# Performance work log

Hardware: AMD Instinct MI355X
Metric: run time of the kernel (lower is better)

The kernel has to match this reference:

```python
import jax, jax.numpy as jnp
import numpy as np

EPS = 1e-08
F_DIM = 512


def setup_inputs() -> dict:
    key = jax.random.key(0)
    ks = jax.random.split(key, 7)
    N, F = 50000, F_DIM
    q = jax.random.normal(ks[0], (N, 1, F), dtype=jnp.float32)
    mu = jax.random.normal(ks[1], (N, 3, F), dtype=jnp.float32)
    # Xavier-ish scaled params
    W_mix = jax.random.normal(ks[2], (2 * F, F), dtype=jnp.float32) * (1.0 / np.sqrt(F))
    W1 = jax.random.normal(ks[3], (F, 2 * F), dtype=jnp.float32) * (1.0 / np.sqrt(2 * F))
    b1 = jnp.zeros((F,), dtype=jnp.float32)
    W2 = jax.random.normal(ks[4], (3 * F, F), dtype=jnp.float32) * (1.0 / np.sqrt(F))
    b2 = jnp.zeros((3 * F,), dtype=jnp.float32)
    return {"q": q, "mu": mu, "W_mix": W_mix, "W1": W1, "b1": b1, "W2": W2, "b2": b2}


def reference(q, mu, W_mix, W1, b1, W2, b2):
    F = q.shape[-1]
    # mu_channel_mix: [N,3,F] @ [F,2F] -> [N,3,2F]
    mu_mix = jnp.einsum('ndf,gf->ndg', mu, W_mix)
    mu_V, mu_W = mu_mix[..., :F], mu_mix[..., F:]
    # vector norm over Cartesian axis -> [N,1,F]
    mu_Vn = jnp.sqrt(jnp.sum(mu_V * mu_V, axis=-2, keepdims=True) + EPS)
    ctx = jnp.concatenate([q, mu_Vn], axis=-1)  # [N,1,2F]
    h = jax.nn.silu(jnp.einsum('nsf,gf->nsg', ctx, W1) + b1)  # [N,1,F]
    x = jnp.einsum('nsf,gf->nsg', h, W2) + b2  # [N,1,3F]
    dq_intra = x[..., :F]
    dmu_intra = x[..., F:2 * F] * mu_W  # broadcast [N,1,F]*[N,3,F]
    dqmu_intra = x[..., 2 * F:] * jnp.sum(mu_V * mu_W, axis=1, keepdims=True)
    q_out = q + dq_intra + dqmu_intra
    mu_out = mu + dmu_intra
    return (q_out, mu_out)
```

## Files before the change

### kernel.cpp

```cpp
#include <hip/hip_runtime.h>
#include <stdint.h>

#define NN 50000
#define QWORDS 25600000

typedef __attribute__((ext_vector_type(8))) short bf16x8;
typedef __attribute__((ext_vector_type(4))) float f32x4;

__device__ __forceinline__ uint32_t f2bf(float x){
  uint32_t u = __builtin_bit_cast(uint32_t, x);
  u += 0x7FFFu + ((u >> 16) & 1u);
  return u >> 16;
}
__device__ __forceinline__ float bf2f(uint32_t b){
  uint32_t u = b << 16;
  return __builtin_bit_cast(float, u);
}
__device__ __forceinline__ void gload16(const uint16_t* g, uint16_t* l){
  __builtin_amdgcn_global_load_lds(
      (const __attribute__((address_space(1))) uint32_t*)g,
      (__attribute__((address_space(3))) uint32_t*)l, 16, 0, 0);
}
__device__ __forceinline__ f32x4 mfma16(bf16x8 a, bf16x8 b, f32x4 c){
  return __builtin_amdgcn_mfma_f32_16x16x32_bf16(a, b, c, 0, 0, 0);
}

#define FENCE() asm volatile("" ::: "memory")

__global__ void k_convert(const float* __restrict__ wmix, const float* __restrict__ w1,
                          const float* __restrict__ w2, uint16_t* __restrict__ dst){
  int i = blockIdx.x * 256 + threadIdx.x;
  int e = i << 2;
  const float* s; int o;
  if (e < 524288)       { s = wmix; o = e; }
  else if (e < 1048576) { s = w1;   o = e - 524288; }
  else                  { s = w2;   o = e - 1048576; }
  f32x4 v = *(const f32x4*)(s + o);
  uint2 pk;
  pk.x = f2bf(v[0]) | (f2bf(v[1]) << 16);
  pk.y = f2bf(v[2]) | (f2bf(v[3]) << 16);
  *(uint2*)(dst + e) = pk;
}

__global__ __launch_bounds__(512, 4)
void k_gemm1(const float* __restrict__ mu, const uint16_t* __restrict__ wmixb,
             uint16_t* __restrict__ qh, float* __restrict__ muW){
  __shared__ uint16_t As[2][12288];
  __shared__ uint16_t Bs[2][8192];
  const int tid  = threadIdx.x;
  const int lane = tid & 63;
  const int w    = tid >> 6;
  const int wn   = w & 3;
  const int wf   = w >> 2;
  const int orig = blockIdx.x;
  const int j    = (orig & 7) * 782 + (orig >> 3);
  const int f0   = (j & 7) * 64;
  const int n0   = (j >> 3) * 64;
  const int lrow = tid >> 4;
  const int lcol = (tid & 15) * 4;

  f32x4 ar[6];
  auto A_LOAD = [&](int ks){
    const int k0 = ks * 64;
    #pragma unroll
    for (int p=0; p<6; ++p){
      int r = p*32 + lrow;
      int d = r >> 6, nrow = r & 63;
      int n = n0 + nrow;
      int g = (n < NN ? n : NN-1)*3 + d;
      ar[p] = *(const f32x4*)(mu + (size_t)g*512 + k0 + lcol);
    }
  };
  auto A_WRITE = [&](int buf){
    #pragma unroll
    for (int p=0; p<6; ++p){
      int r = p*32 + lrow;
      f32x4 v = ar[p];
      uint2 pk;
      pk.x = f2bf(v[0]) | (f2bf(v[1]) << 16);
      pk.y = f2bf(v[2]) | (f2bf(v[3]) << 16);
      *(uint2*)&As[buf][r*64 + (lcol ^ ((r&7)<<3))] = pk;
    }
  };
  auto B_ISSUE = [&](int ks, int buf){
    const int k0 = ks * 64;
    #pragma unroll
    for (int jj=0; jj<2; ++jj){
      int jb = w*2 + jj;
      int row = jb*8 + (lane>>3);
      int g = (row < 64) ? (f0 + row) : (448 + f0 + row);
      int srcc = ((lane&7) ^ ((lane>>3)&7)) * 8;
      gload16(wmixb + (size_t)g*512 + k0 + srcc, &Bs[buf][jb*512]);
    }
  };

  const f32x4 z4 = {0.f,0.f,0.f,0.f};
  f32x4 acc[3][4];
  #pragma unroll
  for (int d=0; d<3; ++d)
    #pragma unroll
    for (int nt=0; nt<4; ++nt) acc[d][nt] = z4;

  A_LOAD(0); B_ISSUE(0, 0); A_WRITE(0);
  for (int ks=0; ks<8; ++ks){
    const int cur = ks & 1;
    __syncthreads();
    if (ks < 7){ A_LOAD(ks+1); B_ISSUE(ks+1, cur^1); }
    #pragma unroll
    for (int kf=0; kf<2; ++kf){
      int kc = kf*32 + (lane>>4)*8;
      bf16x8 af[3];
      #pragma unroll
      for (int d=0; d<3; ++d){
        int r = d*64 + wn*16 + (lane&15);
        af[d] = *(const bf16x8*)&As[cur][r*64 + (kc ^ ((r&7)<<3))];
      }
      #pragma unroll
      for (int nt=0; nt<4; ++nt){
        int ntg = wf*2 + (nt&1) + (nt>>1)*4;
        int rr = ntg*16 + (lane&15);
        bf16x8 bf = *(const bf16x8*)&Bs[cur][rr*64 + (kc ^ ((rr&7)<<3))];
        #pragma unroll
        for (int d=0; d<3; ++d)
          acc[d][nt] = mfma16(bf, af[d], acc[d][nt]);
      }
    }
    if (ks < 7) A_WRITE(cur^1);
  }

  const int rb4 = (lane >> 4) * 4;
  const int nthr = n0 + wn*16 + (lane & 15);
  if (nthr < NN){
    #pragma unroll
    for (int c=0; c<2; ++c){
      int f = f0 + (wf*2 + c)*16 + rb4;
      uint2 pkv, pkd; f32x4 u0v, u1v, u2v;
      uint32_t vb[4], db[4];
      #pragma unroll
      for (int p=0; p<4; ++p){
        float v0 = acc[0][c][p],   v1 = acc[1][c][p],   v2 = acc[2][c][p];
        float u0 = acc[0][c+2][p], u1 = acc[1][c+2][p], u2 = acc[2][c+2][p];
        float vn = sqrtf(v0*v0 + v1*v1 + v2*v2 + 1e-8f);
        float dt = v0*u0 + v1*u1 + v2*u2;
        vb[p] = f2bf(vn); db[p] = f2bf(dt);
        u0v[p] = u0; u1v[p] = u1; u2v[p] = u2;
      }
      pkv.x = vb[0] | (vb[1] << 16); pkv.y = vb[2] | (vb[3] << 16);
      pkd.x = db[0] | (db[1] << 16); pkd.y = db[2] | (db[3] << 16);
      *(uint2*)(qh + (size_t)nthr*1024 + f)       = pkv;
      *(uint2*)(qh + (size_t)nthr*1024 + 512 + f) = pkd;
      size_t mb = (size_t)nthr*1536 + f;
      *(f32x4*)(muW + mb)        = u0v;
      *(f32x4*)(muW + mb + 512)  = u1v;
      *(f32x4*)(muW + mb + 1024) = u2v;
    }
  }
}

__global__ __launch_bounds__(512, 4)
void k_gemm2(const float* __restrict__ q, const uint16_t* __restrict__ w1b,
             const float* __restrict__ b1, uint16_t* __restrict__ qh){
  __shared__ uint16_t A2[2][2048];
  __shared__ uint16_t B2[2][16384];
  const int tid  = threadIdx.x;
  const int lane = tid & 63;
  const int w    = tid >> 6;
  const int wm   = w >> 2;
  const int wn   = w & 3;
  const int n0   = blockIdx.x * 64;

  f32x4 qa;
  auto QA_LOAD = [&](int s){
    int k0 = s*32;
    int row = tid >> 3, ch = tid & 7;
    int nc = (n0 + row < NN) ? n0 + row : NN-1;
    qa = *(const f32x4*)(q + (size_t)nc*512 + k0 + ch*4);
  };
  auto QA_WRITE = [&](int buf){
    int row = tid >> 3, ch = tid & 7;
    uint2 pk;
    pk.x = f2bf(qa[0]) | (f2bf(qa[1]) << 16);
    pk.y = f2bf(qa[2]) | (f2bf(qa[3]) << 16);
    *(uint2*)&A2[buf][row*32 + (((ch>>1) ^ (row&3))<<3) + (ch&1)*4] = pk;
  };
  auto VA_ISSUE = [&](int s, int buf){
    if (w < 4){
      int k0v = (s-16)*32;
      int row = w*16 + (lane>>2);
      int nc = (n0 + row < NN) ? n0 + row : NN-1;
      int srcch = (lane&3) ^ (row&3);
      gload16(qh + (size_t)nc*1024 + k0v + srcch*8, &A2[buf][w*512]);
    }
  };
  auto B_ISSUE = [&](int s, int buf){
    int k0 = s*32;
    #pragma unroll
    for (int jj=0; jj<4; ++jj){
      int j = w*4 + jj;
      int row = j*16 + (lane>>2);
      int srcch = (lane&3) ^ (row&3);
      gload16(w1b + (size_t)row*1024 + k0 + srcch*8, &B2[buf][j*512]);
    }
  };

  const f32x4 z4 = {0.f,0.f,0.f,0.f};
  f32x4 acc2[2][8];
  #pragma unroll
  for (int mt=0; mt<2; ++mt)
    #pragma unroll
    for (int nt=0; nt<8; ++nt) acc2[mt][nt] = z4;

  QA_LOAD(0); B_ISSUE(0, 0); QA_WRITE(0);
  for (int s=0; s<32; ++s){
    const int cur = s & 1;
    __syncthreads();
    if (s < 31){
      if (s+1 < 16) QA_LOAD(s+1); else VA_ISSUE(s+1, cur^1);
      B_ISSUE(s+1, cur^1);
    }
    {
      int kc = (lane>>4)*8;
      bf16x8 a[2];
      #pragma unroll
      for (int mt=0; mt<2; ++mt){
        int r = wm*32 + mt*16 + (lane&15);
        a[mt] = *(const bf16x8*)&A2[cur][r*32 + (kc ^ ((r&3)<<3))];
      }
      #pragma unroll
      for (int nt=0; nt<8; ++nt){
        int rr = wn*128 + nt*16 + (lane&15);
        bf16x8 b = *(const bf16x8*)&B2[cur][rr*32 + (kc ^ ((rr&3)<<3))];
        acc2[0][nt] = mfma16(a[0], b, acc2[0][nt]);
        acc2[1][nt] = mfma16(a[1], b, acc2[1][nt]);
      }
    }
    if (s < 31 && s+1 < 16) QA_WRITE(cur^1);
  }

  const int rb4 = (lane >> 4) * 4;
  #pragma unroll
  for (int nt=0; nt<8; ++nt){
    int col = wn*128 + nt*16 + (lane&15);
    float bb = b1[col];
    #pragma unroll
    for (int mt=0; mt<2; ++mt)
      #pragma unroll
      for (int j=0; j<4; ++j){
        int n = n0 + wm*32 + mt*16 + rb4 + j;
        if (n < NN){
          float x = acc2[mt][nt][j] + bb;
          float sv = x / (1.f + __expf(-x));
          qh[(size_t)n*1024 + col] = (uint16_t)f2bf(sv);
        }
      }
  }
}

__global__ __launch_bounds__(512, 4)
void k_gemm3(const float* __restrict__ q, const float* __restrict__ mu,
             const uint16_t* __restrict__ w2b, const float* __restrict__ b2,
             float* __restrict__ dout){
  __shared__ uint16_t Hs[32*512];
  __shared__ uint16_t B3[2][12288];
  const int tid  = threadIdx.x;
  const int lane = tid & 63;
  const int w    = tid >> 6;
  const int wm   = w >> 2;
  const int wn   = w & 3;
  const int n0   = blockIdx.x * 32;
  const uint16_t* qh = (const uint16_t*)dout;
  float* mout = dout + (size_t)QWORDS;
  const int l15 = lane & 15;
  const int rb4 = (lane >> 4) * 4;
  const f32x4 z4 = {0.f,0.f,0.f,0.f};

  #pragma unroll
  for (int i=0; i<4; ++i){
    int row = w*4 + i;
    int nc = (n0 + row < NN) ? n0 + row : NN-1;
    gload16(qh + (size_t)nc*1024 + (size_t)((lane ^ (row&7))*8), &Hs[row*512]);
  }

  auto B_ISSUE = [&](int it, int ks, uint16_t* slot){
    #pragma unroll
    for (int jj=0; jj<3; ++jj){
      int j = w*3 + jj;
      int rr = j*8 + (lane>>3);
      int s3 = rr >> 6, fi = rr & 63;
      int g = s3*512 + it*64 + fi;
      gload16(w2b + (size_t)g*512 + ks*64 + ((lane&7) ^ (rr&7))*8, slot + j*512);
    }
  };
  B_ISSUE(0, 0, B3[0]);

  const int nthr = n0 + wm*16 + l15;
  const int nc   = nthr < NN ? nthr : NN-1;

  f32x4 qv, bbv[3], muv[3], mwv[3];
  float dtv[4];
  int   fb = 0;
  f32x4 acc3[3];

#define K3_MFMA(KS) do{ \
    const uint16_t* bsl = B3[(KS)&1]; \
    __builtin_amdgcn_s_setprio(1); \
    _Pragma("unroll") \
    for (int kf=0; kf<2; ++kf){ \
      int r = wm*16 + l15; \
      int ch = ((KS)*8 + kf*4 + (lane>>4)) ^ (r&7); \
      bf16x8 a = *(const bf16x8*)&Hs[r*512 + ch*8]; \
      _Pragma("unroll") \
      for (int s3=0; s3<3; ++s3){ \
        int rr = s3*64 + wn*16 + l15; \
        int chb = (kf*4 + (lane>>4)) ^ (rr&7); \
        bf16x8 b = *(const bf16x8*)&bsl[rr*64 + chb*8]; \
        acc3[s3] = mfma16(b, a, acc3[s3]); \
      } \
    } \
    __builtin_amdgcn_s_setprio(0); \
  } while(0)

  #pragma unroll 1
  for (int it=0; it<8; ++it){
    if (it) { asm volatile("s_waitcnt vmcnt(4)" ::: "memory"); }
    else    { asm volatile("s_waitcnt vmcnt(0)" ::: "memory"); }
    __builtin_amdgcn_s_barrier();
    B_ISSUE(it, 1, B3[1]);
    FENCE();
    {
      #pragma unroll
      for (int s3=0; s3<3; ++s3) acc3[s3] = z4;
      fb = it*64 + wn*16 + rb4;
      bbv[0] = *(const f32x4*)(b2 + fb);
      bbv[1] = *(const f32x4*)(b2 + 512 + fb);
      bbv[2] = *(const f32x4*)(b2 + 1024 + fb);
      uint2 du = *(const uint2*)(qh + (size_t)nc*1024 + 512 + fb);
      dtv[0] = bf2f(du.x & 0xffff); dtv[1] = bf2f(du.x >> 16);
      dtv[2] = bf2f(du.y & 0xffff); dtv[3] = bf2f(du.y >> 16);
      qv = *(const f32x4*)(q + (size_t)nc*512 + fb);
    }
    FENCE();
    K3_MFMA(0);

    asm volatile("s_waitcnt vmcnt(5)" ::: "memory");
    __builtin_amdgcn_s_barrier();
    B_ISSUE(it, 2, B3[0]);
    FENCE();
    {
      size_t mb = (size_t)nc*1536 + fb;
      muv[0] = *(const f32x4*)(mu + mb);
      muv[1] = *(const f32x4*)(mu + mb + 512);
      muv[2] = *(const f32x4*)(mu + mb + 1024);
    }
    FENCE();
    K3_MFMA(1);

    asm volatile("s_waitcnt vmcnt(3)" ::: "memory");
    __builtin_amdgcn_s_barrier();
    B_ISSUE(it, 3, B3[1]);
    FENCE();
    {
      size_t mb = (size_t)nc*1536 + fb;
      mwv[0] = *(const f32x4*)(mout + mb);
      mwv[1] = *(const f32x4*)(mout + mb + 512);
      mwv[2] = *(const f32x4*)(mout + mb + 1024);
    }
    FENCE();
    K3_MFMA(2);

    asm volatile("s_waitcnt vmcnt(3)" ::: "memory");
    __builtin_amdgcn_s_barrier();
    B_ISSUE(it, 4, B3[0]);
    FENCE();
    K3_MFMA(3);

    asm volatile("s_waitcnt vmcnt(0)" ::: "memory");
    __builtin_amdgcn_s_barrier();
    B_ISSUE(it, 5, B3[1]);
    FENCE();
    K3_MFMA(4);

    asm volatile("s_waitcnt vmcnt(0)" ::: "memory");
    __builtin_amdgcn_s_barrier();
    B_ISSUE(it, 6, B3[0]);
    FENCE();
    K3_MFMA(5);

    asm volatile("s_waitcnt vmcnt(0)" ::: "memory");
    __builtin_amdgcn_s_barrier();
    B_ISSUE(it, 7, B3[1]);
    FENCE();
    K3_MFMA(6);

    asm volatile("s_waitcnt vmcnt(0)" ::: "memory");
    __builtin_amdgcn_s_barrier();
    if (it < 7) B_ISSUE(it+1, 0, B3[0]);
    FENCE();
    K3_MFMA(7);
    if (nthr < NN){
      f32x4 qo, m0, m1, m2;
      #pragma unroll
      for (int p=0; p<4; ++p){
        float x0 = acc3[0][p] + bbv[0][p];
        float x1 = acc3[1][p] + bbv[1][p];
        float x2 = acc3[2][p] + bbv[2][p];
        qo[p] = qv[p] + x0 + x2*dtv[p];
        m0[p] = muv[0][p] + x1*mwv[0][p];
        m1[p] = muv[1][p] + x1*mwv[1][p];
        m2[p] = muv[2][p] + x1*mwv[2][p];
      }
      *(f32x4*)(dout + (size_t)nthr*512 + fb) = qo;
      size_t mb = (size_t)nthr*1536 + fb;
      *(f32x4*)(mout + mb)        = m0;
      *(f32x4*)(mout + mb + 512)  = m1;
      *(f32x4*)(mout + mb + 1024) = m2;
    }
  }
#undef K3_MFMA
}

extern "C" void kernel_launch(void* const* d_in, const int* in_sizes, int n_in,
                              void* d_out, int out_size, void* d_ws, size_t ws_size,
                              hipStream_t stream){
  (void)in_sizes; (void)n_in; (void)out_size; (void)ws_size;
  const float* q    = (const float*)d_in[0];
  const float* mu   = (const float*)d_in[1];
  const float* wmix = (const float*)d_in[2];
  const float* w1   = (const float*)d_in[3];
  const float* b1   = (const float*)d_in[4];
  const float* w2   = (const float*)d_in[5];
  const float* b2   = (const float*)d_in[6];
  uint16_t* wb = (uint16_t*)d_ws;
  float* dout = (float*)d_out;

  hipLaunchKernelGGL(k_convert, dim3(1792), dim3(256), 0, stream, wmix, w1, w2, wb);
  hipLaunchKernelGGL(k_gemm1, dim3(6256), dim3(512), 0, stream,
                     mu, wb, (uint16_t*)d_out, dout + (size_t)QWORDS);
  hipLaunchKernelGGL(k_gemm2, dim3(782), dim3(512), 0, stream,
                     q, wb + 524288, b1, (uint16_t*)d_out);
  hipLaunchKernelGGL(k_gemm3, dim3(1563), dim3(512), 0, stream,
                     q, mu, wb + 1048576, b2, dout);
}
```

Measured before the change: 898.4 us.

## Pre-convert mu to bf16 and load it asynchronously into LDS in gemm1

Adds a pass that converts mu from fp32 to bf16 in workspace, and a new gemm1 variant that streams the bf16 mu tiles straight into LDS with global_load_lds, as already done for the weights, instead of loading fp32 through registers and converting. The aim is to halve the A-operand bytes read by each of gemm1's many tiles and let the A loads overlap compute. In exchange it adds a full extra read of mu in fp32 plus a write and re-read of the bf16 copy. It only takes effect when the workspace is large enough, otherwise it falls back to the old kernel.

```diff
diff --git a/kernel.cpp b/kernel.cpp
--- a/kernel.cpp
+++ b/kernel.cpp
@@ -36,6 +36,16 @@
   else if (e < 1048576) { s = w1;   o = e - 524288; }
   else                  { s = w2;   o = e - 1048576; }
   f32x4 v = *(const f32x4*)(s + o);
+  uint2 pk;
+  pk.x = f2bf(v[0]) | (f2bf(v[1]) << 16);
+  pk.y = f2bf(v[2]) | (f2bf(v[3]) << 16);
+  *(uint2*)(dst + e) = pk;
+}
+
+__global__ void k_convmu(const float* __restrict__ mu, uint16_t* __restrict__ dst){
+  size_t i = (size_t)blockIdx.x * 256 + threadIdx.x;
+  size_t e = i << 2;
+  f32x4 v = *(const f32x4*)(mu + e);
   uint2 pk;
   pk.x = f2bf(v[0]) | (f2bf(v[1]) << 16);
   pk.y = f2bf(v[2]) | (f2bf(v[3]) << 16);
@@ -126,6 +136,108 @@
       }
     }
     if (ks < 7) A_WRITE(cur^1);
+  }
+
+  const int rb4 = (lane >> 4) * 4;
+  const int nthr = n0 + wn*16 + (lane & 15);
+  if (nthr < NN){
+    #pragma unroll
+    for (int c=0; c<2; ++c){
+      int f = f0 + (wf*2 + c)*16 + rb4;
+      uint2 pkv, pkd; f32x4 u0v, u1v, u2v;
+      uint32_t vb[4], db[4];
+      #pragma unroll
+      for (int p=0; p<4; ++p){
+        float v0 = acc[0][c][p],   v1 = acc[1][c][p],   v2 = acc[2][c][p];
+        float u0 = acc[0][c+2][p], u1 = acc[1][c+2][p], u2 = acc[2][c+2][p];
+        float vn = sqrtf(v0*v0 + v1*v1 + v2*v2 + 1e-8f);
+        float dt = v0*u0 + v1*u1 + v2*u2;
+        vb[p] = f2bf(vn); db[p] = f2bf(dt);
+        u0v[p] = u0; u1v[p] = u1; u2v[p] = u2;
+      }
+      pkv.x = vb[0] | (vb[1] << 16); pkv.y = vb[2] | (vb[3] << 16);
+      pkd.x = db[0] | (db[1] << 16); pkd.y = db[2] | (db[3] << 16);
+      *(uint2*)(qh + (size_t)nthr*1024 + f)       = pkv;
+      *(uint2*)(qh + (size_t)nthr*1024 + 512 + f) = pkd;
+      size_t mb = (size_t)nthr*1536 + f;
+      *(f32x4*)(muW + mb)        = u0v;
+      *(f32x4*)(muW + mb + 512)  = u1v;
+      *(f32x4*)(muW + mb + 1024) = u2v;
+    }
+  }
+}
+
+__global__ __launch_bounds__(512, 4)
+void k_gemm1b(const uint16_t* __restrict__ mu16, const uint16_t* __restrict__ wmixb,
+              uint16_t* __restrict__ qh, float* __restrict__ muW){
+  __shared__ uint16_t As[2][12288];
+  __shared__ uint16_t Bs[2][8192];
+  const int tid  = threadIdx.x;
+  const int lane = tid & 63;
+  const int w    = tid >> 6;
+  const int wn   = w & 3;
+  const int wf   = w >> 2;
+  const int orig = blockIdx.x;
+  const int j    = (orig & 7) * 782 + (orig >> 3);
+  const int f0   = (j & 7) * 64;
+  const int n0   = (j >> 3) * 64;
+
+  auto A_ISSUE = [&](int ks, int buf){
+    const int k0 = ks * 64;
+    #pragma unroll
+    for (int jj=0; jj<3; ++jj){
+      int jb = w*3 + jj;
+      int rr = jb*8 + (lane>>3);
+      int d = rr >> 6, nrow = rr & 63;
+      int n = n0 + nrow;
+      int g = (n < NN ? n : NN-1)*3 + d;
+      int srcc = ((lane&7) ^ ((lane>>3)&7)) * 8;
+      gload16(mu16 + (size_t)g*512 + k0 + srcc, &As[buf][jb*512]);
+    }
+  };
+  auto B_ISSUE = [&](int ks, int buf){
+    const int k0 = ks * 64;
+    #pragma unroll
+    for (int jj=0; jj<2; ++jj){
+      int jb = w*2 + jj;
+      int row = jb*8 + (lane>>3);
+      int g = (row < 64) ? (f0 + row) : (448 + f0 + row);
+      int srcc = ((lane&7) ^ ((lane>>3)&7)) * 8;
+      gload16(wmixb + (size_t)g*512 + k0 + srcc, &Bs[buf][jb*512]);
+    }
+  };
+
+  const f32x4 z4 = {0.f,0.f,0.f,0.f};
+  f32x4 acc[3][4];
+  #pragma unroll
+  for (int d=0; d<3; ++d)
+    #pragma unroll
+    for (int nt=0; nt<4; ++nt) acc[d][nt] = z4;
+
+  A_ISSUE(0, 0); B_ISSUE(0, 0);
+  for (int ks=0; ks<8; ++ks){
+    const int cur = ks & 1;
+    __syncthreads();
+    if (ks < 7){ A_ISSUE(ks+1, cur^1); B_ISSUE(ks+1, cur^1); }
+    #pragma unroll
+    for (int kf=0; kf<2; ++kf){
+      int kc = kf*32 + (lane>>4)*8;
+      bf16x8 af[3];
+      #pragma unroll
+      for (int d=0; d<3; ++d){
+        int r = d*64 + wn*16 + (lane&15);
+        af[d] = *(const bf16x8*)&As[cur][r*64 + (kc ^ ((r&7)<<3))];
+      }
+      #pragma unroll
+      for (int nt=0; nt<4; ++nt){
+        int ntg = wf*2 + (nt&1) + (nt>>1)*4;
+        int rr = ntg*16 + (lane&15);
+        bf16x8 bf = *(const bf16x8*)&Bs[cur][rr*64 + (kc ^ ((rr&7)<<3))];
+        #pragma unroll
+        for (int d=0; d<3; ++d)
+          acc[d][nt] = mfma16(bf, af[d], acc[d][nt]);
+      }
+    }
   }
 
   const int rb4 = (lane >> 4) * 4;
@@ -422,7 +534,7 @@
 extern "C" void kernel_launch(void* const* d_in, const int* in_sizes, int n_in,
                               void* d_out, int out_size, void* d_ws, size_t ws_size,
                               hipStream_t stream){
-  (void)in_sizes; (void)n_in; (void)out_size; (void)ws_size;
+  (void)in_sizes; (void)n_in; (void)out_size;
   const float* q    = (const float*)d_in[0];
   const float* mu   = (const float*)d_in[1];
   const float* wmix = (const float*)d_in[2];
@@ -434,8 +546,18 @@
   float* dout = (float*)d_out;
 
   hipLaunchKernelGGL(k_convert, dim3(1792), dim3(256), 0, stream, wmix, w1, w2, wb);
-  hipLaunchKernelGGL(k_gemm1, dim3(6256), dim3(512), 0, stream,
-                     mu, wb, (uint16_t*)d_out, dout + (size_t)QWORDS);
+
+  const size_t need = ((size_t)1835008 + (size_t)NN*1536) * 2;
+  if (ws_size >= need){
+    uint16_t* mu16 = wb + 1835008;
+    hipLaunchKernelGGL(k_convmu, dim3(75000), dim3(256), 0, stream, mu, mu16);
+    hipLaunchKernelGGL(k_gemm1b, dim3(6256), dim3(512), 0, stream,
+                       mu16, wb, (uint16_t*)d_out, dout + (size_t)QWORDS);
+  } else {
+    hipLaunchKernelGGL(k_gemm1, dim3(6256), dim3(512), 0, stream,
+                       mu, wb, (uint16_t*)d_out, dout + (size_t)QWORDS);
+  }
+
   hipLaunchKernelGGL(k_gemm2, dim3(782), dim3(512), 0, stream,
                      q, wb + 524288, b1, (uint16_t*)d_out);
   hipLaunchKernelGGL(k_gemm3, dim3(1563), dim3(512), 0, stream,
```

New measurement: 916.3 us. Within noise of the previous version (+2.0%).
